# Performance work log

Measured on AMD Instinct MI355X. Metric: run time of the kernel, lower is better.

Reference implementation:

```python
import jax, jax.numpy as jnp
import numpy as np

EPS = 1e-5

def _mvn(feat):
    # instance-norm style mean/std over spatial dims; torch .var is unbiased (ddof=1)
    b, c = feat.shape[:2]
    flat = feat.reshape(b, c, -1)
    mu = flat.mean(-1)[:, :, None, None]
    std = jnp.sqrt(flat.var(-1, ddof=1) + EPS)[:, :, None, None]
    return (feat - mu) / std

def setup_inputs() -> dict:
    key = jax.random.key(0)
    ks = jax.random.split(key, 10)
    B, C, H, W = 4, 512, 64, 64
    sc = 0.05
    return {
        "content": jax.random.normal(ks[0], (B, C, H, W), jnp.float32),
        "style": jax.random.normal(ks[1], (B, C, H, W), jnp.float32),
        "content_key": jax.random.normal(ks[2], (B, C, H, W), jnp.float32),
        "style_key": jax.random.normal(ks[3], (B, C, H, W), jnp.float32),
        "Wf": jax.random.normal(ks[4], (C, C), jnp.float32) * sc,
        "bf": jax.random.normal(ks[5], (C,), jnp.float32) * sc,
        "Wg": jax.random.normal(ks[6], (C, C), jnp.float32) * sc,
        "bg": jax.random.normal(ks[7], (C,), jnp.float32) * sc,
        "Wh": jax.random.normal(ks[8], (C, C), jnp.float32) * sc,
        "bh": jax.random.normal(ks[9], (C,), jnp.float32) * sc,
    }

def reference(content, style, content_key, style_key, Wf, bf, Wg, bg, Wh, bh):
    b, C, h, w = content.shape
    hs, ws = style.shape[2], style.shape[3]
    n, m = h * w, hs * ws
    # 1x1 convs are per-pixel linear maps
    Fq = jnp.einsum('oc,bcn->bno', Wf, content_key.reshape(b, -1, n)) + bf      # [b, n, ck]
    G = jnp.einsum('oc,bcn->bon', Wg, style_key.reshape(b, -1, m)) + bg[:, None]  # [b, ck, m]
    V = jnp.einsum('oc,bcn->bno', Wh, style.reshape(b, C, m)) + bh              # [b, m, C]
    S = jax.nn.softmax(jnp.einsum('bnc,bcm->bnm', Fq, G), axis=-1)              # [b, n, m]
    mean = jnp.einsum('bnm,bmc->bnc', S, V)                                     # attention-weighted mean
    m2 = jnp.einsum('bnm,bmc->bnc', S, V * V)                                   # weighted second moment
    std = jnp.sqrt(jax.nn.relu(m2 - mean * mean))
    mean = mean.reshape(b, h, w, C).transpose(0, 3, 1, 2)
    std = std.reshape(b, h, w, C).transpose(0, 3, 1, 2)
    return std * _mvn(content) + mean
```

## Files before the change

### kernel.cpp

```cpp
#include <hip/hip_runtime.h>
#include <math.h>

#define BATCH 4
#define C 512
#define N 4096
#define M 4096
#define MSPLIT 4

typedef __attribute__((ext_vector_type(8))) short short8;
typedef __attribute__((ext_vector_type(8))) __bf16 bf16x8;
typedef __attribute__((ext_vector_type(4))) float f32x4;

static __device__ __forceinline__ unsigned short f2bf(float x) {
    unsigned u = __float_as_uint(x);
    u += 0x7fff + ((u >> 16) & 1);
    return (unsigned short)(u >> 16);
}
static __device__ __forceinline__ float bf2f(unsigned short h) {
    return __uint_as_float(((unsigned)h) << 16);
}
static __device__ __forceinline__ f32x4 mfma_bf16(short8 a, short8 b, f32x4 c) {
    return __builtin_amdgcn_mfma_f32_16x16x32_bf16(
        __builtin_bit_cast(bf16x8, a), __builtin_bit_cast(bf16x8, b), c, 0, 0, 0);
}
static __device__ __forceinline__ void gload16(const void* g, void* l) {
    __builtin_amdgcn_global_load_lds(
        (const __attribute__((address_space(1))) void*)g,
        (__attribute__((address_space(3))) void*)l, 16, 0, 0);
}

__global__ __launch_bounds__(256) void wsplit_kernel(
    const float* __restrict__ W, unsigned short* __restrict__ hi,
    unsigned short* __restrict__ lo)
{
    int i = blockIdx.x * 256 + threadIdx.x;
    float v = W[i];
    unsigned short h = f2bf(v);
    hi[i] = h;
    lo[i] = f2bf(v - bf2f(h));
}

__global__ __launch_bounds__(256) void linear_fg_mfma(
    const float* __restrict__ in,
    const unsigned short* __restrict__ Whi, const unsigned short* __restrict__ Wlo,
    const float* __restrict__ bias,
    unsigned short* __restrict__ out_hi, unsigned short* __restrict__ out_lo)
{
    __shared__ float in_s[32][68];
    __shared__ __align__(16) unsigned short wh_s[64][40];
    __shared__ __align__(16) unsigned short wl_s[64][40];
    const int tid = threadIdx.x;
    const int n0 = blockIdx.x * 64, o0 = blockIdx.y * 64;
    const int w = tid >> 6, lane = tid & 63;
    const int wrow = w >> 1, wcol = w & 1;
    const int lr = lane & 15, q = lane >> 4;
    f32x4 acc[2][2];
    #pragma unroll
    for (int i = 0; i < 2; ++i)
        #pragma unroll
        for (int j = 0; j < 2; ++j) acc[i][j] = (f32x4){0.f, 0.f, 0.f, 0.f};

    for (int kc = 0; kc < C; kc += 32) {
        __syncthreads();
        #pragma unroll
        for (int it = 0; it < 2; ++it) {
            int idx = tid + it * 256;
            int k = idx >> 4, seg = idx & 15;
            *(float4*)&in_s[k][seg * 4] =
                *(const float4*)&in[(size_t)(kc + k) * N + n0 + seg * 4];
        }
        {
            int o = tid >> 2, sg = tid & 3;
            *(float4*)&wh_s[o][sg * 8] = *(const float4*)&Whi[(size_t)(o0 + o) * 512 + kc + sg * 8];
            *(float4*)&wl_s[o][sg * 8] = *(const float4*)&Wlo[(size_t)(o0 + o) * 512 + kc + sg * 8];
        }
        __syncthreads();
        short8 ah[2], al[2], bh[2], bl[2];
        #pragma unroll
        for (int i = 0; i < 2; ++i) {
            int n = wrow * 32 + i * 16 + lr;
            #pragma unroll
            for (int j = 0; j < 8; ++j) {
                float f = in_s[q * 8 + j][n];
                unsigned short h = f2bf(f);
                ah[i][j] = (short)h;
                al[i][j] = (short)f2bf(f - bf2f(h));
            }
        }
        #pragma unroll
        for (int j = 0; j < 2; ++j) {
            int o = wcol * 32 + j * 16 + lr;
            bh[j] = *(const short8*)&wh_s[o][q * 8];
            bl[j] = *(const short8*)&wl_s[o][q * 8];
        }
        #pragma unroll
        for (int i = 0; i < 2; ++i)
            #pragma unroll
            for (int j = 0; j < 2; ++j) {
                acc[i][j] = mfma_bf16(ah[i], bh[j], acc[i][j]);
                acc[i][j] = mfma_bf16(ah[i], bl[j], acc[i][j]);
                acc[i][j] = mfma_bf16(al[i], bh[j], acc[i][j]);
            }
    }
    #pragma unroll
    for (int i = 0; i < 2; ++i)
        #pragma unroll
        for (int j = 0; j < 2; ++j) {
            int o = o0 + wcol * 32 + j * 16 + lr;
            float bo = bias[o];
            #pragma unroll
            for (int r = 0; r < 4; ++r) {
                int n = n0 + wrow * 32 + i * 16 + q * 4 + r;
                float v = acc[i][j][r] + bo;
                unsigned short h = f2bf(v);
                out_hi[(size_t)n * 512 + o] = h;
                out_lo[(size_t)n * 512 + o] = f2bf(v - bf2f(h));
            }
        }
}

__global__ __launch_bounds__(256) void linear_v_mfma(
    const float* __restrict__ in,
    const unsigned short* __restrict__ Whi, const unsigned short* __restrict__ Wlo,
    const float* __restrict__ bias,
    unsigned short* __restrict__ vhT, unsigned short* __restrict__ v2hT,
    unsigned short* __restrict__ v2lT)
{
    __shared__ float in_s[32][68];
    __shared__ __align__(16) unsigned short wh_s[64][40];
    __shared__ __align__(16) unsigned short wl_s[64][40];
    const int tid = threadIdx.x;
    const int m0 = blockIdx.x * 64, o0 = blockIdx.y * 64;
    const int w = tid >> 6, lane = tid & 63;
    const int wrow = w >> 1, wcol = w & 1;
    const int lr = lane & 15, q = lane >> 4;
    f32x4 acc[2][2];
    #pragma unroll
    for (int i = 0; i < 2; ++i)
        #pragma unroll
        for (int j = 0; j < 2; ++j) acc[i][j] = (f32x4){0.f, 0.f, 0.f, 0.f};

    for (int kc = 0; kc < C; kc += 32) {
        __syncthreads();
        #pragma unroll
        for (int it = 0; it < 2; ++it) {
            int idx = tid + it * 256;
            int k = idx >> 4, seg = idx & 15;
            *(float4*)&in_s[k][seg * 4] =
                *(const float4*)&in[(size_t)(kc + k) * N + m0 + seg * 4];
        }
        {
            int o = tid >> 2, sg = tid & 3;
            *(float4*)&wh_s[o][sg * 8] = *(const float4*)&Whi[(size_t)(o0 + o) * 512 + kc + sg * 8];
            *(float4*)&wl_s[o][sg * 8] = *(const float4*)&Wlo[(size_t)(o0 + o) * 512 + kc + sg * 8];
        }
        __syncthreads();
        short8 ah[2], al[2], bh[2], bl[2];
        #pragma unroll
        for (int i = 0; i < 2; ++i) {
            int o = wrow * 32 + i * 16 + lr;
            ah[i] = *(const short8*)&wh_s[o][q * 8];
            al[i] = *(const short8*)&wl_s[o][q * 8];
        }
        #pragma unroll
        for (int j = 0; j < 2; ++j) {
            int m = wcol * 32 + j * 16 + lr;
            #pragma unroll
            for (int t = 0; t < 8; ++t) {
                float f = in_s[q * 8 + t][m];
                unsigned short h = f2bf(f);
                bh[j][t] = (short)h;
                bl[j][t] = (short)f2bf(f - bf2f(h));
            }
        }
        #pragma unroll
        for (int i = 0; i < 2; ++i)
            #pragma unroll
            for (int j = 0; j < 2; ++j) {
                acc[i][j] = mfma_bf16(ah[i], bh[j], acc[i][j]);
                acc[i][j] = mfma_bf16(ah[i], bl[j], acc[i][j]);
                acc[i][j] = mfma_bf16(al[i], bh[j], acc[i][j]);
            }
    }
    #pragma unroll
    for (int i = 0; i < 2; ++i)
        #pragma unroll
        for (int r = 0; r < 4; ++r) {
            int o = o0 + wrow * 32 + i * 16 + q * 4 + r;
            float bo = bias[o];
            #pragma unroll
            for (int j = 0; j < 2; ++j) {
                int m = m0 + wcol * 32 + j * 16 + lr;
                float v = acc[i][j][r] + bo;
                unsigned short vh = f2bf(v);
                float vhf = bf2f(vh);
                float vsq = vhf * vhf;
                unsigned short v2h = f2bf(vsq);
                unsigned short v2l = f2bf(vsq - bf2f(v2h));
                size_t off = (size_t)o * M + m;
                vhT[off] = vh;
                v2hT[off] = v2h;
                v2lT[off] = v2l;
            }
        }
}

__global__ __launch_bounds__(256) void logits_mfma_kernel(
    const unsigned short* __restrict__ Ah, const unsigned short* __restrict__ Al,
    const unsigned short* __restrict__ Bh, const unsigned short* __restrict__ Bl,
    float* __restrict__ S)
{
    __shared__ __align__(16) unsigned short Ah_s[128 * 32];
    __shared__ __align__(16) unsigned short Al_s[128 * 32];
    __shared__ __align__(16) unsigned short Bh_s[128 * 32];
    __shared__ __align__(16) unsigned short Bl_s[128 * 32];
    const int tid = threadIdx.x;
    const int n0 = blockIdx.y * 128, m0 = blockIdx.x * 128;
    const int w = tid >> 6, lane = tid & 63;
    const int wrow = w >> 1, wcol = w & 1;
    const int lr = lane & 15, q = lane >> 4;
    const int srow = lane >> 2, scol = (lane & 3) * 8;
    f32x4 acc[4][4];
    #pragma unroll
    for (int i = 0; i < 4; ++i)
        #pragma unroll
        for (int j = 0; j < 4; ++j)
            acc[i][j] = (f32x4){0.f, 0.f, 0.f, 0.f};

    for (int kc = 0; kc < C; kc += 32) {
        __syncthreads();
        #pragma unroll
        for (int g2 = 0; g2 < 2; ++g2) {
            int g = w * 2 + g2;
            size_t ga = (size_t)(n0 + g * 16 + srow) * C + kc + scol;
            size_t gb = (size_t)(m0 + g * 16 + srow) * C + kc + scol;
            int lo = g * 512;
            gload16(&Ah[ga], &Ah_s[lo]);
            gload16(&Al[ga], &Al_s[lo]);
            gload16(&Bh[gb], &Bh_s[lo]);
            gload16(&Bl[gb], &Bl_s[lo]);
        }
        __syncthreads();
        short8 ah[4], al[4], bh[4], bl[4];
        #pragma unroll
        for (int i = 0; i < 4; ++i) {
            int ro = (wrow * 64 + i * 16 + lr) * 32 + q * 8;
            int co = (wcol * 64 + i * 16 + lr) * 32 + q * 8;
            ah[i] = *(const short8*)&Ah_s[ro];
            al[i] = *(const short8*)&Al_s[ro];
            bh[i] = *(const short8*)&Bh_s[co];
            bl[i] = *(const short8*)&Bl_s[co];
        }
        #pragma unroll
        for (int i = 0; i < 4; ++i)
            #pragma unroll
            for (int j = 0; j < 4; ++j) {
                acc[i][j] = mfma_bf16(ah[i], bh[j], acc[i][j]);
                acc[i][j] = mfma_bf16(ah[i], bl[j], acc[i][j]);
                acc[i][j] = mfma_bf16(al[i], bh[j], acc[i][j]);
            }
    }
    #pragma unroll
    for (int i = 0; i < 4; ++i) {
        int nb = n0 + wrow * 64 + i * 16 + q * 4;
        #pragma unroll
        for (int j = 0; j < 4; ++j) {
            int m = m0 + wcol * 64 + j * 16 + lr;
            #pragma unroll
            for (int r = 0; r < 4; ++r)
                S[(size_t)(nb + r) * M + m] = acc[i][j][r];
        }
    }
}

__global__ __launch_bounds__(256) void rowstat_p_kernel(
    const float* __restrict__ S, unsigned short* __restrict__ P,
    float* __restrict__ rsum)
{
    const int n = blockIdx.x;
    const int tid = threadIdx.x;
    const float* row = S + (size_t)n * M;
    float v[16];
    #pragma unroll
    for (int i = 0; i < 16; ++i) v[i] = row[tid + i * 256];
    float lm = -INFINITY;
    #pragma unroll
    for (int i = 0; i < 16; ++i) lm = fmaxf(lm, v[i]);
    #pragma unroll
    for (int off = 32; off > 0; off >>= 1) lm = fmaxf(lm, __shfl_xor(lm, off, 64));
    __shared__ float red[4];
    __shared__ float redsum[4];
    const int wid = tid >> 6, lane = tid & 63;
    if (lane == 0) red[wid] = lm;
    __syncthreads();
    const float rm = fmaxf(fmaxf(red[0], red[1]), fmaxf(red[2], red[3]));
    float ls = 0.f;
    unsigned short* prow = P + (size_t)n * M;
    #pragma unroll
    for (int i = 0; i < 16; ++i) {
        float p = __expf(v[i] - rm);
        unsigned short pb = f2bf(p);
        prow[tid + i * 256] = pb;
        ls += bf2f(pb);
    }
    #pragma unroll
    for (int off = 32; off > 0; off >>= 1) ls += __shfl_xor(ls, off, 64);
    if (lane == 0) redsum[wid] = ls;
    __syncthreads();
    if (tid == 0) rsum[n] = redsum[0] + redsum[1] + redsum[2] + redsum[3];
}

__global__ __launch_bounds__(256) void apply_partial_kernel(
    const unsigned short* __restrict__ P, const unsigned short* __restrict__ VhT,
    const unsigned short* __restrict__ V2hT, const unsigned short* __restrict__ V2lT,
    float* __restrict__ accm_p, float* __restrict__ acc2_p)
{
    __shared__ __align__(16) unsigned short P_s[2][128 * 32];
    __shared__ __align__(16) unsigned short Vh_s[2][64 * 32];
    __shared__ __align__(16) unsigned short V2h_s[2][64 * 32];
    __shared__ __align__(16) unsigned short V2l_s[2][64 * 32];
    const int tid = threadIdx.x;
    const int bid = blockIdx.x;
    const int xcd = bid & 7, j = bid >> 3;
    const int c0 = (j & 7) * 64;
    const int gl = j >> 3;
    const int z  = gl >> 2;
    const int n0 = (xcd * 4 + (gl & 3)) * 128;
    const int w = tid >> 6, lane = tid & 63;
    const int wrow = w >> 1, wcol = w & 1;
    const int lr = lane & 15, q = lane >> 4;
    const int srow = lane >> 2, scol = (lane & 3) * 8;
    f32x4 accm[4][2], acc2[4][2];
    #pragma unroll
    for (int i = 0; i < 4; ++i)
        #pragma unroll
        for (int j2 = 0; j2 < 2; ++j2) {
            accm[i][j2] = (f32x4){0.f, 0.f, 0.f, 0.f};
            acc2[i][j2] = (f32x4){0.f, 0.f, 0.f, 0.f};
        }

    const int mbeg = z * (M / MSPLIT);
    const size_t vrow  = (size_t)(c0 + w * 16 + srow) * M + scol;
    const size_t prow0 = (size_t)(n0 + (w * 2)     * 16 + srow) * M + scol;
    const size_t prow1 = (size_t)(n0 + (w * 2 + 1) * 16 + srow) * M + scol;

    auto STAGE = [&](int buf, int mc) {
        gload16(&P[prow0 + mc],    &P_s[buf][(w * 2)     * 512]);
        gload16(&P[prow1 + mc],    &P_s[buf][(w * 2 + 1) * 512]);
        gload16(&VhT [vrow + mc],  &Vh_s[buf][w * 512]);
        gload16(&V2hT[vrow + mc],  &V2h_s[buf][w * 512]);
        gload16(&V2lT[vrow + mc],  &V2l_s[buf][w * 512]);
    };

    const int NT = (M / MSPLIT) / 32;
    STAGE(0, mbeg);
    STAGE(1, mbeg + 32);

    for (int t = 0; t < NT; ++t) {
        if (t < NT - 1) asm volatile("s_waitcnt vmcnt(5)" ::: "memory");
        else            asm volatile("s_waitcnt vmcnt(0)" ::: "memory");
        __builtin_amdgcn_sched_barrier(0);
        __builtin_amdgcn_s_barrier();
        __builtin_amdgcn_sched_barrier(0);
        const int cur = t & 1;
        short8 a[4], bh[2], b2h[2], b2l[2];
        #pragma unroll
        for (int i = 0; i < 4; ++i)
            a[i] = *(const short8*)&P_s[cur][(wrow * 64 + i * 16 + lr) * 32 + q * 8];
        #pragma unroll
        for (int j2 = 0; j2 < 2; ++j2) {
            int off = (wcol * 32 + j2 * 16 + lr) * 32 + q * 8;
            bh[j2]  = *(const short8*)&Vh_s[cur][off];
            b2h[j2] = *(const short8*)&V2h_s[cur][off];
            b2l[j2] = *(const short8*)&V2l_s[cur][off];
        }
        __builtin_amdgcn_s_setprio(1);
        #pragma unroll
        for (int i = 0; i < 4; ++i)
            #pragma unroll
            for (int j2 = 0; j2 < 2; ++j2) {
                accm[i][j2] = mfma_bf16(a[i], bh[j2],  accm[i][j2]);
                acc2[i][j2] = mfma_bf16(a[i], b2h[j2], acc2[i][j2]);
                acc2[i][j2] = mfma_bf16(a[i], b2l[j2], acc2[i][j2]);
            }
        __builtin_amdgcn_s_setprio(0);
        __builtin_amdgcn_sched_barrier(0);
        __builtin_amdgcn_s_barrier();
        __builtin_amdgcn_sched_barrier(0);
        if (t + 2 < NT) STAGE(cur, mbeg + (t + 2) * 32);
    }

    const size_t pbase = (size_t)z * N * C;
    #pragma unroll
    for (int i = 0; i < 4; ++i) {
        int nb = n0 + wrow * 64 + i * 16 + q * 4;
        #pragma unroll
        for (int j2 = 0; j2 < 2; ++j2) {
            int c = c0 + wcol * 32 + j2 * 16 + lr;
            #pragma unroll
            for (int r = 0; r < 4; ++r) {
                size_t off = pbase + (size_t)(nb + r) * C + c;
                accm_p[off] = accm[i][j2][r];
                acc2_p[off] = acc2[i][j2][r];
            }
        }
    }
}

__global__ __launch_bounds__(256) void combine_kernel(
    const float* __restrict__ accm_p, const float* __restrict__ acc2_p,
    const float* __restrict__ rsum, float* __restrict__ meanw,
    float* __restrict__ stdw)
{
    const size_t idx = ((size_t)blockIdx.x * 256 + threadIdx.x) * 4;
    const int n = (int)(idx >> 9);
    const float inv = 1.0f / rsum[n];
    float sm[4] = {0.f, 0.f, 0.f, 0.f}, s2[4] = {0.f, 0.f, 0.f, 0.f};
    #pragma unroll
    for (int z = 0; z < MSPLIT; ++z) {
        float4 a = *(const float4*)&accm_p[(size_t)z * N * C + idx];
        float4 b = *(const float4*)&acc2_p[(size_t)z * N * C + idx];
        sm[0] += a.x; sm[1] += a.y; sm[2] += a.z; sm[3] += a.w;
        s2[0] += b.x; s2[1] += b.y; s2[2] += b.z; s2[3] += b.w;
    }
    float4 mnv, sdv;
    float* mp = (float*)&mnv;
    float* sp = (float*)&sdv;
    #pragma unroll
    for (int k = 0; k < 4; ++k) {
        float mn = sm[k] * inv;
        float m2 = s2[k] * inv;
        mp[k] = mn;
        sp[k] = sqrtf(fmaxf(m2 - mn * mn, 0.f));
    }
    *(float4*)&meanw[idx] = mnv;
    *(float4*)&stdw[idx]  = sdv;
}

__global__ __launch_bounds__(256) void mvn_kernel(
    const float* __restrict__ content, float* __restrict__ mu, float* __restrict__ rstd)
{
    const int c = blockIdx.x;
    const int tid = threadIdx.x;
    const float* row = content + (size_t)c * N;
    float s = 0.f, ss = 0.f;
    for (int i = tid; i < N; i += 256) {
        float v = row[i];
        s += v;
        ss = fmaf(v, v, ss);
    }
    #pragma unroll
    for (int off = 32; off > 0; off >>= 1) {
        s  += __shfl_xor(s,  off, 64);
        ss += __shfl_xor(ss, off, 64);
    }
    __shared__ float rs[4], rss[4];
    const int wid = tid >> 6, lane = tid & 63;
    if (lane == 0) { rs[wid] = s; rss[wid] = ss; }
    __syncthreads();
    if (tid == 0) {
        float st = rs[0] + rs[1] + rs[2] + rs[3];
        float sst = rss[0] + rss[1] + rss[2] + rss[3];
        float m = st / (float)N;
        float var = (sst - st * st / (float)N) / (float)(N - 1);
        mu[c] = m;
        rstd[c] = rsqrtf(var + 1e-5f);
    }
}

__global__ __launch_bounds__(256) void final_kernel(
    const float* __restrict__ content, const float* __restrict__ meanw,
    const float* __restrict__ stdw, const float* __restrict__ mu,
    const float* __restrict__ rstd, float* __restrict__ out)
{
    __shared__ float mn_s[32][33], sd_s[32][33];
    const int tid = threadIdx.x;
    const int n0 = blockIdx.x * 32;
    const int c0 = blockIdx.y * 32;
    const int tx = tid & 31, ty = tid >> 5;
    #pragma unroll
    for (int i = 0; i < 4; ++i) {
        int n = ty + i * 8;
        mn_s[tx][n] = meanw[(size_t)(n0 + n) * C + c0 + tx];
        sd_s[tx][n] = stdw [(size_t)(n0 + n) * C + c0 + tx];
    }
    __syncthreads();
    #pragma unroll
    for (int i = 0; i < 4; ++i) {
        int c = ty + i * 8;
        float m = mu[c0 + c], r = rstd[c0 + c];
        size_t off = (size_t)(c0 + c) * N + n0 + tx;
        float x = content[off];
        out[off] = sd_s[c][tx] * (x - m) * r + mn_s[c][tx];
    }
}

extern "C" void kernel_launch(void* const* d_in, const int* in_sizes, int n_in,
                              void* d_out, int out_size, void* d_ws, size_t ws_size,
                              hipStream_t stream)
{
    const float* content = (const float*)d_in[0];
    const float* style   = (const float*)d_in[1];
    const float* ckey    = (const float*)d_in[2];
    const float* skey    = (const float*)d_in[3];
    const float* Wf      = (const float*)d_in[4];
    const float* bf      = (const float*)d_in[5];
    const float* Wg      = (const float*)d_in[6];
    const float* bg      = (const float*)d_in[7];
    const float* Wh      = (const float*)d_in[8];
    const float* bh      = (const float*)d_in[9];
    float* out = (float*)d_out;

    const size_t sz_w  = (size_t)512 * 512 * 2;
    const size_t sz_S  = (size_t)N * M * 4;
    const size_t sz_FG = (size_t)N * C * 2;
    const size_t sz_P  = (size_t)N * M * 2;
    const size_t sz_V  = (size_t)C * M * 2;

    char* p = (char*)d_ws;
    auto alloc = [&](size_t bytes) {
        char* r = p;
        p += (bytes + 255) & ~(size_t)255;
        return r;
    };
    unsigned short* WfH = (unsigned short*)alloc(sz_w);
    unsigned short* WfL = (unsigned short*)alloc(sz_w);
    unsigned short* WgH = (unsigned short*)alloc(sz_w);
    unsigned short* WgL = (unsigned short*)alloc(sz_w);
    unsigned short* WhH = (unsigned short*)alloc(sz_w);
    unsigned short* WhL = (unsigned short*)alloc(sz_w);
    float* S = (float*)alloc(sz_S);
    unsigned short* Fh = (unsigned short*)alloc(sz_FG);
    unsigned short* Fl = (unsigned short*)alloc(sz_FG);
    unsigned short* Gh = (unsigned short*)alloc(sz_FG);
    unsigned short* Gl = (unsigned short*)alloc(sz_FG);
    unsigned short* P    = (unsigned short*)alloc(sz_P);
    unsigned short* VhT  = (unsigned short*)alloc(sz_V);
    unsigned short* V2hT = (unsigned short*)alloc(sz_V);
    unsigned short* V2lT = (unsigned short*)alloc(sz_V);
    float* rsum  = (float*)alloc((size_t)N * 4);
    float* meanw = (float*)alloc((size_t)N * C * 4);
    float* stdw  = (float*)alloc((size_t)N * C * 4);
    float* mu    = (float*)alloc((size_t)C * 4);
    float* rstd  = (float*)alloc((size_t)C * 4);

    float* accm_p = S;
    float* acc2_p = S + (size_t)MSPLIT * N * C;

    wsplit_kernel<<<dim3(1024), 256, 0, stream>>>(Wf, WfH, WfL);
    wsplit_kernel<<<dim3(1024), 256, 0, stream>>>(Wg, WgH, WgL);
    wsplit_kernel<<<dim3(1024), 256, 0, stream>>>(Wh, WhH, WhL);

    for (int b = 0; b < BATCH; ++b) {
        const size_t fo = (size_t)b * C * N;
        linear_fg_mfma<<<dim3(N / 64, C / 64), 256, 0, stream>>>(ckey + fo, WfH, WfL, bf, Fh, Fl);
        linear_fg_mfma<<<dim3(M / 64, C / 64), 256, 0, stream>>>(skey + fo, WgH, WgL, bg, Gh, Gl);
        linear_v_mfma<<<dim3(M / 64, C / 64), 256, 0, stream>>>(style + fo, WhH, WhL, bh,
                                                                VhT, V2hT, V2lT);
        logits_mfma_kernel<<<dim3(M / 128, N / 128), 256, 0, stream>>>(Fh, Fl, Gh, Gl, S);
        rowstat_p_kernel<<<dim3(N), 256, 0, stream>>>(S, P, rsum);
        apply_partial_kernel<<<dim3(1024), 256, 0, stream>>>(
            P, VhT, V2hT, V2lT, accm_p, acc2_p);
        combine_kernel<<<dim3(N * C / 1024), 256, 0, stream>>>(
            accm_p, acc2_p, rsum, meanw, stdw);
        mvn_kernel<<<dim3(C), 256, 0, stream>>>(content + fo, mu, rstd);
        final_kernel<<<dim3(N / 32, C / 32), 256, 0, stream>>>(
            content + fo, meanw, stdw, mu, rstd, out + fo);
    }
}
```

Measured before the change: 1.101 ms.

## Pre-split and transpose projection inputs to bf16 hi/lo, load via global_load_lds

Adds a kernel that transposes content_key, style_key and style into n-major layout and splits each value into bf16 hi/lo parts once per batch, storing them in spare space at the end of the S buffer. The three projection GEMMs then stage their operands straight into LDS with direct global-to-LDS loads instead of converting fp32 columns in the inner loop. The aim is to stop repeating the hi/lo split for every output-channel tile, which happened eight times per input. The cost is an extra pass that writes and rereads the split inputs, and it relies on S not being live while the projections run.

```diff
diff --git a/kernel.cpp b/kernel.cpp
--- a/kernel.cpp
+++ b/kernel.cpp
@@ -40,20 +40,67 @@
     lo[i] = f2bf(v - bf2f(h));
 }
 
-__global__ __launch_bounds__(256) void linear_fg_mfma(
-    const float* __restrict__ in,
+__global__ __launch_bounds__(256) void xsplit3_t_kernel(
+    const float* __restrict__ in0, const float* __restrict__ in1,
+    const float* __restrict__ in2,
+    unsigned short* __restrict__ h0, unsigned short* __restrict__ l0,
+    unsigned short* __restrict__ h1, unsigned short* __restrict__ l1,
+    unsigned short* __restrict__ h2, unsigned short* __restrict__ l2)
+{
+    __shared__ float ls[64][65];
+    const int tid = threadIdx.x;
+    const int n0 = blockIdx.x * 64, c0 = blockIdx.y * 64;
+    const float* ins[3] = {in0, in1, in2};
+    unsigned short* hs[3] = {h0, h1, h2};
+    unsigned short* los[3] = {l0, l1, l2};
+    #pragma unroll
+    for (int t = 0; t < 3; ++t) {
+        const float* in = ins[t];
+        __syncthreads();
+        #pragma unroll
+        for (int p = 0; p < 4; ++p) {
+            int c = p * 16 + (tid >> 4);
+            int n = (tid & 15) * 4;
+            *(float4*)&ls[c][n] = *(const float4*)&in[(size_t)(c0 + c) * N + n0 + n];
+        }
+        __syncthreads();
+        unsigned short* hp = hs[t];
+        unsigned short* lp = los[t];
+        #pragma unroll
+        for (int p = 0; p < 2; ++p) {
+            int n = p * 32 + (tid >> 3);
+            int c = (tid & 7) * 8;
+            short8 vh, vl;
+            #pragma unroll
+            for (int e = 0; e < 8; ++e) {
+                float f = ls[c + e][n];
+                unsigned short h = f2bf(f);
+                vh[e] = (short)h;
+                vl[e] = (short)f2bf(f - bf2f(h));
+            }
+            size_t off = (size_t)(n0 + n) * C + c0 + c;
+            *(short8*)&hp[off] = vh;
+            *(short8*)&lp[off] = vl;
+        }
+    }
+}
+
+__global__ __launch_bounds__(256) void linear_fg2_mfma(
+    const unsigned short* __restrict__ Xh, const unsigned short* __restrict__ Xl,
     const unsigned short* __restrict__ Whi, const unsigned short* __restrict__ Wlo,
     const float* __restrict__ bias,
     unsigned short* __restrict__ out_hi, unsigned short* __restrict__ out_lo)
 {
-    __shared__ float in_s[32][68];
-    __shared__ __align__(16) unsigned short wh_s[64][40];
-    __shared__ __align__(16) unsigned short wl_s[64][40];
+    __shared__ __align__(16) unsigned short Ah_s[64 * 32];
+    __shared__ __align__(16) unsigned short Al_s[64 * 32];
+    __shared__ __align__(16) unsigned short Bh_s[64 * 32];
+    __shared__ __align__(16) unsigned short Bl_s[64 * 32];
     const int tid = threadIdx.x;
     const int n0 = blockIdx.x * 64, o0 = blockIdx.y * 64;
     const int w = tid >> 6, lane = tid & 63;
     const int wrow = w >> 1, wcol = w & 1;
     const int lr = lane & 15, q = lane >> 4;
+    const int srow = lane >> 2, scol = (lane & 3) * 8;
     f32x4 acc[2][2];
     #pragma unroll
     for (int i = 0; i < 2; ++i)
@@ -62,36 +109,27 @@
 
     for (int kc = 0; kc < C; kc += 32) {
         __syncthreads();
-        #pragma unroll
-        for (int it = 0; it < 2; ++it) {
-            int idx = tid + it * 256;
-            int k = idx >> 4, seg = idx & 15;
-            *(float4*)&in_s[k][seg * 4] =
-                *(const float4*)&in[(size_t)(kc + k) * N + n0 + seg * 4];
-        }
         {
-            int o = tid >> 2, sg = tid & 3;
-            *(float4*)&wh_s[o][sg * 8] = *(const float4*)&Whi[(size_t)(o0 + o) * 512 + kc + sg * 8];
-            *(float4*)&wl_s[o][sg * 8] = *(const float4*)&Wlo[(size_t)(o0 + o) * 512 + kc + sg * 8];
+            size_t ga = (size_t)(n0 + w * 16 + srow) * C + kc + scol;
+            size_t gb = (size_t)(o0 + w * 16 + srow) * 512 + kc + scol;
+            gload16(&Xh[ga],  &Ah_s[w * 512]);
+            gload16(&Xl[ga],  &Al_s[w * 512]);
+            gload16(&Whi[gb], &Bh_s[w * 512]);
+            gload16(&Wlo[gb], &Bl_s[w * 512]);
         }
         __syncthreads();
         short8 ah[2], al[2], bh[2], bl[2];
         #pragma unroll
         for (int i = 0; i < 2; ++i) {
-            int n = wrow * 32 + i * 16 + lr;
-            #pragma unroll
-            for (int j = 0; j < 8; ++j) {
-                float f = in_s[q * 8 + j][n];
-                unsigned short h = f2bf(f);
-                ah[i][j] = (short)h;
-                al[i][j] = (short)f2bf(f - bf2f(h));
-            }
+            int ro = (wrow * 32 + i * 16 + lr) * 32 + q * 8;
+            ah[i] = *(const short8*)&Ah_s[ro];
+            al[i] = *(const short8*)&Al_s[ro];
         }
         #pragma unroll
         for (int j = 0; j < 2; ++j) {
-            int o = wcol * 32 + j * 16 + lr;
-            bh[j] = *(const short8*)&wh_s[o][q * 8];
-            bl[j] = *(const short8*)&wl_s[o][q * 8];
+            int co = (wcol * 32 + j * 16 + lr) * 32 + q * 8;
+            bh[j] = *(const short8*)&Bh_s[co];
+            bl[j] = *(const short8*)&Bl_s[co];
         }
         #pragma unroll
         for (int i = 0; i < 2; ++i)
@@ -119,21 +157,23 @@
         }
 }
 
-__global__ __launch_bounds__(256) void linear_v_mfma(
-    const float* __restrict__ in,
+__global__ __launch_bounds__(256) void linear_v2_mfma(
+    const unsigned short* __restrict__ Sh, const unsigned short* __restrict__ Sl,
     const unsigned short* __restrict__ Whi, const unsigned short* __restrict__ Wlo,
     const float* __restrict__ bias,
     unsigned short* __restrict__ vhT, unsigned short* __restrict__ v2hT,
     unsigned short* __restrict__ v2lT)
 {
-    __shared__ float in_s[32][68];
-    __shared__ __align__(16) unsigned short wh_s[64][40];
-    __shared__ __align__(16) unsigned short wl_s[64][40];
+    __shared__ __align__(16) unsigned short Ah_s[64 * 32];
+    __shared__ __align__(16) unsigned short Al_s[64 * 32];
+    __shared__ __align__(16) unsigned short Bh_s[64 * 32];
+    __shared__ __align__(16) unsigned short Bl_s[64 * 32];
     const int tid = threadIdx.x;
     const int m0 = blockIdx.x * 64, o0 = blockIdx.y * 64;
     const int w = tid >> 6, lane = tid & 63;
     const int wrow = w >> 1, wcol = w & 1;
     const int lr = lane & 15, q = lane >> 4;
+    const int srow = lane >> 2, scol = (lane & 3) * 8;
     f32x4 acc[2][2];
     #pragma unroll
     for (int i = 0; i < 2; ++i)
@@ -142,36 +182,27 @@
 
     for (int kc = 0; kc < C; kc += 32) {
         __syncthreads();
-        #pragma unroll
-        for (int it = 0; it < 2; ++it) {
-            int idx = tid + it * 256;
-            int k = idx >> 4, seg = idx & 15;
-            *(float4*)&in_s[k][seg * 4] =
-                *(const float4*)&in[(size_t)(kc + k) * N + m0 + seg * 4];
-        }
         {
-            int o = tid >> 2, sg = tid & 3;
-            *(float4*)&wh_s[o][sg * 8] = *(const float4*)&Whi[(size_t)(o0 + o) * 512 + kc + sg * 8];
-            *(float4*)&wl_s[o][sg * 8] = *(const float4*)&Wlo[(size_t)(o0 + o) * 512 + kc + sg * 8];
+            size_t ga = (size_t)(o0 + w * 16 + srow) * 512 + kc + scol;
+            size_t gb = (size_t)(m0 + w * 16 + srow) * C + kc + scol;
+            gload16(&Whi[ga], &Ah_s[w * 512]);
+            gload16(&Wlo[ga], &Al_s[w * 512]);
+            gload16(&Sh[gb],  &Bh_s[w * 512]);
+            gload16(&Sl[gb],  &Bl_s[w * 512]);
         }
         __syncthreads();
         short8 ah[2], al[2], bh[2], bl[2];
         #pragma unroll
         for (int i = 0; i < 2; ++i) {
-            int o = wrow * 32 + i * 16 + lr;
-            ah[i] = *(const short8*)&wh_s[o][q * 8];
-            al[i] = *(const short8*)&wl_s[o][q * 8];
+            int ro = (wrow * 32 + i * 16 + lr) * 32 + q * 8;
+            ah[i] = *(const short8*)&Ah_s[ro];
+            al[i] = *(const short8*)&Al_s[ro];
         }
         #pragma unroll
         for (int j = 0; j < 2; ++j) {
-            int m = wcol * 32 + j * 16 + lr;
-            #pragma unroll
-            for (int t = 0; t < 8; ++t) {
-                float f = in_s[q * 8 + t][m];
-                unsigned short h = f2bf(f);
-                bh[j][t] = (short)h;
-                bl[j][t] = (short)f2bf(f - bf2f(h));
-            }
+            int co = (wcol * 32 + j * 16 + lr) * 32 + q * 8;
+            bh[j] = *(const short8*)&Bh_s[co];
+            bl[j] = *(const short8*)&Bl_s[co];
         }
         #pragma unroll
         for (int i = 0; i < 2; ++i)
@@ -516,6 +547,7 @@
     const size_t sz_FG = (size_t)N * C * 2;
     const size_t sz_P  = (size_t)N * M * 2;
     const size_t sz_V  = (size_t)C * M * 2;
+    const size_t sz_X  = (size_t)N * C * 2;
 
     char* p = (char*)d_ws;
     auto alloc = [&](size_t bytes) {
@@ -547,16 +579,28 @@
     float* accm_p = S;
     float* acc2_p = S + (size_t)MSPLIT * N * C;
 
+    char* xbase = (char*)S + (sz_S - 6 * sz_X);
+    unsigned short* CkH = (unsigned short*)(xbase + 0 * sz_X);
+    unsigned short* CkL = (unsigned short*)(xbase + 1 * sz_X);
+    unsigned short* SkH = (unsigned short*)(xbase + 2 * sz_X);
+    unsigned short* SkL = (unsigned short*)(xbase + 3 * sz_X);
+    unsigned short* StH = (unsigned short*)(xbase + 4 * sz_X);
+    unsigned short* StL = (unsigned short*)(xbase + 5 * sz_X);
+
     wsplit_kernel<<<dim3(1024), 256, 0, stream>>>(Wf, WfH, WfL);
     wsplit_kernel<<<dim3(1024), 256, 0, stream>>>(Wg, WgH, WgL);
     wsplit_kernel<<<dim3(1024), 256, 0, stream>>>(Wh, WhH, WhL);
 
     for (int b = 0; b < BATCH; ++b) {
         const size_t fo = (size_t)b * C * N;
-        linear_fg_mfma<<<dim3(N / 64, C / 64), 256, 0, stream>>>(ckey + fo, WfH, WfL, bf, Fh, Fl);
-        linear_fg_mfma<<<dim3(M / 64, C / 64), 256, 0, stream>>>(skey + fo, WgH, WgL, bg, Gh, Gl);
-        linear_v_mfma<<<dim3(M / 64, C / 64), 256, 0, stream>>>(style + fo, WhH, WhL, bh,
-                                                                VhT, V2hT, V2lT);
+        xsplit3_t_kernel<<<dim3(N / 64, C / 64), 256, 0, stream>>>(
+            ckey + fo, skey + fo, style + fo, CkH, CkL, SkH, SkL, StH, StL);
+        linear_fg2_mfma<<<dim3(N / 64, C / 64), 256, 0, stream>>>(
+            CkH, CkL, WfH, WfL, bf, Fh, Fl);
+        linear_fg2_mfma<<<dim3(M / 64, C / 64), 256, 0, stream>>>(
+            SkH, SkL, WgH, WgL, bg, Gh, Gl);
+        linear_v2_mfma<<<dim3(M / 64, C / 64), 256, 0, stream>>>(
+            StH, StL, WhH, WhL, bh, VhT, V2hT, V2lT);
         logits_mfma_kernel<<<dim3(M / 128, N / 128), 256, 0, stream>>>(Fh, Fl, Gh, Gl, S);
         rowstat_p_kernel<<<dim3(N), 256, 0, stream>>>(S, P, rsum);
         apply_partial_kernel<<<dim3(1024), 256, 0, stream>>>(
```

Measured after the change: 1.018 ms. 7.5% less time.
